# Performance work log

Measured on AMD Instinct MI355X. Metric: run time of the kernel, lower is better.

The kernel has to match this reference:

```python
import jax, jax.numpy as jnp
import numpy as np

N = 100000          # number of nodes (queries == sources here)
DEG = 32            # uniform neighbor count
E = N * DEG         # total edges
C_IN = 8
HID = 32
C_OUT = 32


def setup_inputs() -> dict:
    key = jax.random.key(0)
    k1, k2, k3, k4, k5 = jax.random.split(key, 5)
    in_features = jax.random.normal(k1, (N, C_IN), dtype=jnp.float32)
    in_weights = jax.random.uniform(k2, (N,), dtype=jnp.float32)
    # MLP: Linear(2*C_IN -> HID), GELU, Linear(HID -> C_OUT)
    W1 = jax.random.normal(k3, (2 * C_IN, HID), dtype=jnp.float32) / np.sqrt(2 * C_IN)
    b1 = jnp.zeros((HID,), dtype=jnp.float32)
    W2 = jax.random.normal(k4, (HID, C_OUT), dtype=jnp.float32) / np.sqrt(HID)
    b2 = jnp.zeros((C_OUT,), dtype=jnp.float32)
    neighbor_index = jax.random.randint(k5, (E,), 0, N, dtype=jnp.int64)
    row_splits = (jnp.arange(N + 1, dtype=jnp.int64) * DEG)  # uniform CSR splits
    return {"in_features": in_features, "in_weights": in_weights,
            "W1": W1, "b1": b1, "W2": W2, "b2": b2,
            "neighbor_index": neighbor_index, "row_splits": row_splits}


def reference(in_features, in_weights, W1, b1, W2, b2, neighbor_index, row_splits):
    num_edges = neighbor_index.shape[0]
    num_out = row_splits.shape[0] - 1  # M output nodes
    # segment id of each edge (== repeat_interleave of node ids by row counts)
    seg = jnp.searchsorted(row_splits, jnp.arange(num_edges), side="right") - 1
    gathered = in_features[neighbor_index]          # [E, C_in] neighbor gather
    self_feats = in_features[seg]                   # [E, C_in] repeated self features
    agg = jnp.concatenate([gathered, self_feats], axis=1)  # [E, 2*C_in]
    h = jax.nn.gelu(agg @ W1 + b1)                  # [E, HID]
    h = h @ W2 + b2                                 # [E, C_out]
    h = in_weights[neighbor_index][:, None] * h     # quadrature weighting
    sums = jax.ops.segment_sum(h, seg, num_segments=num_out)  # segment_csr sum
    counts = (row_splits[1:] - row_splits[:-1]).astype(h.dtype)
    out = sums / jnp.maximum(counts, 1)[:, None]    # reduce='mean'
    return out
```

## Files before the change

kernel.cpp:

```cpp
#include <hip/hip_runtime.h>

#define DEG 32
#define HID 32
#define CIN 8

typedef float v2f __attribute__((ext_vector_type(2)));

#define GELU_A ((float)(2.0 * 1.4426950408889634 * 0.7978845608028654))
#define GELU_B ((float)(2.0 * 1.4426950408889634 * 0.7978845608028654 * 0.044715))

__device__ __forceinline__ unsigned f2bf(float f) {
    unsigned b = __float_as_uint(f);
    return (b + 0x7fffu + ((b >> 16) & 1u)) >> 16;
}

__global__ __launch_bounds__(256) void precompute_u16(
    const float* __restrict__ x, const float* __restrict__ W1,
    unsigned* __restrict__ u16, int N) {
    int tid = blockIdx.x * 256 + threadIdx.x;
    if (tid >= N * 4) return;
    int n = tid >> 2;
    int q = tid & 3;
    const float4* xp = (const float4*)(x + (size_t)n * CIN);
    float4 a = xp[0], b = xp[1];
    float xv[8] = {a.x, a.y, a.z, a.w, b.x, b.y, b.z, b.w};
    float s[8];
#pragma unroll
    for (int c = 0; c < 8; ++c) s[c] = 0.f;
#pragma unroll
    for (int k = 0; k < 8; ++k) {
        float4 w0 = *(const float4*)(W1 + k * HID + q * 8);
        float4 w1 = *(const float4*)(W1 + k * HID + q * 8 + 4);
        s[0] = fmaf(xv[k], w0.x, s[0]); s[1] = fmaf(xv[k], w0.y, s[1]);
        s[2] = fmaf(xv[k], w0.z, s[2]); s[3] = fmaf(xv[k], w0.w, s[3]);
        s[4] = fmaf(xv[k], w1.x, s[4]); s[5] = fmaf(xv[k], w1.y, s[5]);
        s[6] = fmaf(xv[k], w1.z, s[6]); s[7] = fmaf(xv[k], w1.w, s[7]);
    }
    uint4 o;
    o.x = f2bf(s[0]) | (f2bf(s[1]) << 16);
    o.y = f2bf(s[2]) | (f2bf(s[3]) << 16);
    o.z = f2bf(s[4]) | (f2bf(s[5]) << 16);
    o.w = f2bf(s[6]) | (f2bf(s[7]) << 16);
    *(uint4*)(u16 + (size_t)n * 16 + q * 4) = o;
}

__global__ __launch_bounds__(256) void git_main3(
    const unsigned* __restrict__ u16, const float* __restrict__ x,
    const float* __restrict__ wgt, const float* __restrict__ W1,
    const float* __restrict__ b1, const float* __restrict__ W2,
    const float* __restrict__ b2, const int* __restrict__ nbr,
    float* __restrict__ out, int N) {
    __shared__ float sW2[HID * HID];
    __shared__ float sb2[HID];

    int t = threadIdx.x;
#pragma unroll
    for (int i = 0; i < 4; ++i) sW2[t + i * 256] = W2[t + i * 256];
    if (t < HID) sb2[t] = b2[t];

    int c2   = t & 15;
    int s    = (t >> 4) & 1;
    int slot = t >> 5;
    int node = blockIdx.x * 8 + slot;
    bool valid = node < N;
    int nc = valid ? node : (N - 1);

    int   j_own = nbr[nc * DEG + (t & 31)];
    int   off_l = j_own << 6;
    float w_own = wgt[j_own];

    float ws = w_own;
    ws += __shfl_xor(ws, 1);  ws += __shfl_xor(ws, 2);
    ws += __shfl_xor(ws, 4);  ws += __shfl_xor(ws, 8);
    ws += __shfl_xor(ws, 16);

    const float4* xip = (const float4*)(x + (size_t)nc * CIN);
    float4 xa = xip[0], xb = xip[1];
    float xs[8] = {xa.x, xa.y, xa.z, xa.w, xb.x, xb.y, xb.z, xb.w};
    v2f vb = *(const v2f*)(b1 + c2 * 2);
#pragma unroll
    for (int k = 0; k < 8; ++k) {
        v2f wcol = *(const v2f*)(W1 + (8 + k) * HID + c2 * 2);
        vb += xs[k] * wcol;
    }

    __syncthreads();

    const char* ub = (const char*)u16;
    int mybyte = c2 * 4;
    unsigned bits[16];
    float    wes[16];
#pragma unroll
    for (int e = 0; e < 16; ++e) {
        int src = 2 * e + s;
        int off = __shfl(off_l, src, 32);
        wes[e]  = __shfl(w_own, src, 32);
        bits[e] = *(const unsigned*)(ub + (unsigned)(off + mybyte));
    }

    v2f g = {0.f, 0.f};
#pragma unroll
    for (int e = 0; e < 16; ++e) {
        unsigned bb = bits[e];
        v2f uf;
        uf.x = __uint_as_float(bb << 16);
        uf.y = __uint_as_float(bb & 0xffff0000u);
        v2f tt = uf + vb;
        v2f x2 = tt * tt;
        v2f zz = tt * (x2 * GELU_B + GELU_A);
        v2f ee;
        ee.x = __builtin_amdgcn_exp2f(zz.x);
        ee.y = __builtin_amdgcn_exp2f(zz.y);
        v2f dd = ee + 1.0f;
        v2f rr;
        rr.x = __builtin_amdgcn_rcpf(dd.x);
        rr.y = __builtin_amdgcn_rcpf(dd.y);
        v2f gl = tt - tt * rr;
        g += wes[e] * gl;
    }

    g.x += __shfl_xor(g.x, 16);
    g.y += __shfl_xor(g.y, 16);

    v2f acc = {0.f, 0.f};
#pragma unroll
    for (int hh = 0; hh < 16; ++hh) {
        int h = s * 16 + hh;
        int srcl = s * 8 + (hh >> 1);
        float gh = (hh & 1) ? __shfl(g.y, srcl, 32) : __shfl(g.x, srcl, 32);
        v2f wrow = *(const v2f*)(sW2 + h * HID + c2 * 2);
        acc += gh * wrow;
    }
    acc.x += __shfl_xor(acc.x, 16);
    acc.y += __shfl_xor(acc.y, 16);

    if (valid && s == 0) {
        v2f bb2 = *(const v2f*)(sb2 + c2 * 2);
        v2f res = (acc + ws * bb2) * (1.0f / DEG);
        *(v2f*)(out + (size_t)node * HID + c2 * 2) = res;
    }
}

__global__ __launch_bounds__(256) void fused_fallback(
    const float* __restrict__ x, const float* __restrict__ wgt,
    const float* __restrict__ W1, const float* __restrict__ b1,
    const float* __restrict__ W2, const float* __restrict__ b2,
    const int* __restrict__ nbr, float* __restrict__ out, int N) {
    __shared__ float sW2[HID * HID];
    __shared__ float sb2[HID];
    __shared__ int2  sp[8 * DEG];
    int t = threadIdx.x;
#pragma unroll
    for (int i = 0; i < 4; ++i) sW2[t + i * 256] = W2[t + i * 256];
    if (t < HID) sb2[t] = b2[t];
    int slot = t >> 5, hid = t & 31;
    int node = blockIdx.x * 8 + slot;
    bool valid = node < N;
    int nc = valid ? node : (N - 1);
    int   j_own = nbr[nc * DEG + hid];
    float w_own = wgt[j_own];
    sp[slot * DEG + hid] = make_int2(j_own * (CIN * 4), __float_as_int(w_own));
    const float4* xip = (const float4*)(x + (size_t)nc * CIN);
    float4 xa = xip[0], xb = xip[1];
    float w1t[8];
#pragma unroll
    for (int k = 0; k < 8; ++k) w1t[k] = W1[k * HID + hid];
    float vb = b1[hid];
    vb = fmaf(xa.x, W1[ 8 * HID + hid], vb);
    vb = fmaf(xa.y, W1[ 9 * HID + hid], vb);
    vb = fmaf(xa.z, W1[10 * HID + hid], vb);
    vb = fmaf(xa.w, W1[11 * HID + hid], vb);
    vb = fmaf(xb.x, W1[12 * HID + hid], vb);
    vb = fmaf(xb.y, W1[13 * HID + hid], vb);
    vb = fmaf(xb.z, W1[14 * HID + hid], vb);
    vb = fmaf(xb.w, W1[15 * HID + hid], vb);
    float ws = w_own;
    ws += __shfl_xor(ws, 1);  ws += __shfl_xor(ws, 2);
    ws += __shfl_xor(ws, 4);  ws += __shfl_xor(ws, 8);
    ws += __shfl_xor(ws, 16);
    __syncthreads();
    const char* xbytes = (const char*)x;
    const int2* myp = &sp[slot * DEG];
    float g = 0.f;
#pragma unroll 8
    for (int e = 0; e < DEG; ++e) {
        int2  p  = myp[e];
        float wj = __int_as_float(p.y);
        const float4* xjp = (const float4*)(xbytes + (unsigned)p.x);
        float4 a = xjp[0], b = xjp[1];
        float tin = vb;
        tin = fmaf(a.x, w1t[0], tin); tin = fmaf(a.y, w1t[1], tin);
        tin = fmaf(a.z, w1t[2], tin); tin = fmaf(a.w, w1t[3], tin);
        tin = fmaf(b.x, w1t[4], tin); tin = fmaf(b.y, w1t[5], tin);
        tin = fmaf(b.z, w1t[6], tin); tin = fmaf(b.w, w1t[7], tin);
        float x2 = tin * tin;
        float z  = tin * fmaf(GELU_B, x2, GELU_A);
        float e2 = __builtin_amdgcn_exp2f(z);
        float r  = __builtin_amdgcn_rcpf(1.0f + e2);
        g = fmaf(wj, fmaf(-tin, r, tin), g);
    }
    float acc = 0.f;
#pragma unroll
    for (int h = 0; h < HID; ++h) {
        float gh = __shfl(g, h, 32);
        acc = fmaf(gh, sW2[h * HID + hid], acc);
    }
    if (valid) out[(size_t)node * HID + hid] = fmaf(ws, sb2[hid], acc) * (1.0f / DEG);
}

extern "C" void kernel_launch(void* const* d_in, const int* in_sizes, int n_in,
                              void* d_out, int out_size, void* d_ws, size_t ws_size,
                              hipStream_t stream) {
    const float* x   = (const float*)d_in[0];
    const float* wq  = (const float*)d_in[1];
    const float* W1  = (const float*)d_in[2];
    const float* b1  = (const float*)d_in[3];
    const float* W2  = (const float*)d_in[4];
    const float* b2  = (const float*)d_in[5];
    const int*   nbr = (const int*)d_in[6];
    float* out = (float*)d_out;

    int N = in_sizes[1];
    size_t need = (size_t)N * 64;

    if (ws_size >= need) {
        unsigned* u16 = (unsigned*)d_ws;
        int blocks_pre = (N * 4 + 255) / 256;
        precompute_u16<<<blocks_pre, 256, 0, stream>>>(x, W1, u16, N);
        int blocks_main = (N + 7) / 8;
        git_main3<<<blocks_main, 256, 0, stream>>>(u16, x, wq, W1, b1, W2, b2, nbr, out, N);
    } else {
        int blocks = (N + 7) / 8;
        fused_fallback<<<blocks, 256, 0, stream>>>(x, wq, W1, b1, W2, b2, nbr, out, N);
    }
}
```

Baseline: 132.3 us.

## Precompute self-projection per node and restructure gather to 8-byte loads via LDS

The prepass now also computes the self-feature half of the first layer plus bias (v = x·W1[8:16] + b1) per node in fp32 and stores it in the workspace, so the main kernel only loads it instead of recomputing it. The main kernel reworks the lane mapping: each lane handles 4 hidden channels for 8 edges and gathers 8-byte bf16 chunks, with neighbor offsets and weights passed through LDS instead of shuffles. The reduced g vector is staged in shared memory for the second-layer matmul, and launch bounds request 8 blocks per SM. In exchange the workspace needs an extra 128 bytes per node, which adds write and read traffic, and there are more cross-lane reductions.

Result: no change. 133.0 us (+0.6%).

```diff
diff --git a/kernel.cpp b/kernel.cpp
--- a/kernel.cpp
+++ b/kernel.cpp
@@ -14,9 +14,10 @@
     return (b + 0x7fffu + ((b >> 16) & 1u)) >> 16;
 }
 
-__global__ __launch_bounds__(256) void precompute_u16(
+__global__ __launch_bounds__(256) void precompute_uv16(
     const float* __restrict__ x, const float* __restrict__ W1,
-    unsigned* __restrict__ u16, int N) {
+    const float* __restrict__ b1, unsigned* __restrict__ u16,
+    float* __restrict__ v32, int N) {
     int tid = blockIdx.x * 256 + threadIdx.x;
     if (tid >= N * 4) return;
     int n = tid >> 2;
@@ -24,120 +25,140 @@
     const float4* xp = (const float4*)(x + (size_t)n * CIN);
     float4 a = xp[0], b = xp[1];
     float xv[8] = {a.x, a.y, a.z, a.w, b.x, b.y, b.z, b.w};
-    float s[8];
-#pragma unroll
-    for (int c = 0; c < 8; ++c) s[c] = 0.f;
+    float4 b1a = *(const float4*)(b1 + q * 8);
+    float4 b1b = *(const float4*)(b1 + q * 8 + 4);
+    float su[8] = {0.f, 0.f, 0.f, 0.f, 0.f, 0.f, 0.f, 0.f};
+    float sv[8] = {b1a.x, b1a.y, b1a.z, b1a.w, b1b.x, b1b.y, b1b.z, b1b.w};
 #pragma unroll
     for (int k = 0; k < 8; ++k) {
-        float4 w0 = *(const float4*)(W1 + k * HID + q * 8);
-        float4 w1 = *(const float4*)(W1 + k * HID + q * 8 + 4);
-        s[0] = fmaf(xv[k], w0.x, s[0]); s[1] = fmaf(xv[k], w0.y, s[1]);
-        s[2] = fmaf(xv[k], w0.z, s[2]); s[3] = fmaf(xv[k], w0.w, s[3]);
-        s[4] = fmaf(xv[k], w1.x, s[4]); s[5] = fmaf(xv[k], w1.y, s[5]);
-        s[6] = fmaf(xv[k], w1.z, s[6]); s[7] = fmaf(xv[k], w1.w, s[7]);
+        float4 u0 = *(const float4*)(W1 + k * HID + q * 8);
+        float4 u1 = *(const float4*)(W1 + k * HID + q * 8 + 4);
+        float4 v0 = *(const float4*)(W1 + (k + 8) * HID + q * 8);
+        float4 v1 = *(const float4*)(W1 + (k + 8) * HID + q * 8 + 4);
+        float xk = xv[k];
+        su[0] = fmaf(xk, u0.x, su[0]); su[1] = fmaf(xk, u0.y, su[1]);
+        su[2] = fmaf(xk, u0.z, su[2]); su[3] = fmaf(xk, u0.w, su[3]);
+        su[4] = fmaf(xk, u1.x, su[4]); su[5] = fmaf(xk, u1.y, su[5]);
+        su[6] = fmaf(xk, u1.z, su[6]); su[7] = fmaf(xk, u1.w, su[7]);
+        sv[0] = fmaf(xk, v0.x, sv[0]); sv[1] = fmaf(xk, v0.y, sv[1]);
+        sv[2] = fmaf(xk, v0.z, sv[2]); sv[3] = fmaf(xk, v0.w, sv[3]);
+        sv[4] = fmaf(xk, v1.x, sv[4]); sv[5] = fmaf(xk, v1.y, sv[5]);
+        sv[6] = fmaf(xk, v1.z, sv[6]); sv[7] = fmaf(xk, v1.w, sv[7]);
     }
     uint4 o;
-    o.x = f2bf(s[0]) | (f2bf(s[1]) << 16);
-    o.y = f2bf(s[2]) | (f2bf(s[3]) << 16);
-    o.z = f2bf(s[4]) | (f2bf(s[5]) << 16);
-    o.w = f2bf(s[6]) | (f2bf(s[7]) << 16);
+    o.x = f2bf(su[0]) | (f2bf(su[1]) << 16);
+    o.y = f2bf(su[2]) | (f2bf(su[3]) << 16);
+    o.z = f2bf(su[4]) | (f2bf(su[5]) << 16);
+    o.w = f2bf(su[6]) | (f2bf(su[7]) << 16);
     *(uint4*)(u16 + (size_t)n * 16 + q * 4) = o;
-}
-
-__global__ __launch_bounds__(256) void git_main3(
-    const unsigned* __restrict__ u16, const float* __restrict__ x,
-    const float* __restrict__ wgt, const float* __restrict__ W1,
-    const float* __restrict__ b1, const float* __restrict__ W2,
+    *(float4*)(v32 + (size_t)n * HID + q * 8)     = make_float4(sv[0], sv[1], sv[2], sv[3]);
+    *(float4*)(v32 + (size_t)n * HID + q * 8 + 4) = make_float4(sv[4], sv[5], sv[6], sv[7]);
+}
+
+__global__ __launch_bounds__(256, 8) void git_main4(
+    const unsigned* __restrict__ u16, const float* __restrict__ v32,
+    const float* __restrict__ wgt, const float* __restrict__ W2,
     const float* __restrict__ b2, const int* __restrict__ nbr,
     float* __restrict__ out, int N) {
     __shared__ float sW2[HID * HID];
     __shared__ float sb2[HID];
+    __shared__ int2  sp[8 * 33];
+    __shared__ float sg[8 * HID];
 
     int t = threadIdx.x;
 #pragma unroll
     for (int i = 0; i < 4; ++i) sW2[t + i * 256] = W2[t + i * 256];
     if (t < HID) sb2[t] = b2[t];
 
-    int c2   = t & 15;
-    int s    = (t >> 4) & 1;
     int slot = t >> 5;
+    int l5   = t & 31;
+    int ep   = l5 >> 3;
+    int c4   = l5 & 7;
     int node = blockIdx.x * 8 + slot;
     bool valid = node < N;
     int nc = valid ? node : (N - 1);
 
-    int   j_own = nbr[nc * DEG + (t & 31)];
-    int   off_l = j_own << 6;
+    int   j_own = nbr[nc * DEG + l5];
     float w_own = wgt[j_own];
+    sp[slot * 33 + l5] = make_int2(j_own << 6, __float_as_int(w_own));
 
     float ws = w_own;
     ws += __shfl_xor(ws, 1);  ws += __shfl_xor(ws, 2);
     ws += __shfl_xor(ws, 4);  ws += __shfl_xor(ws, 8);
     ws += __shfl_xor(ws, 16);
 
-    const float4* xip = (const float4*)(x + (size_t)nc * CIN);
-    float4 xa = xip[0], xb = xip[1];
-    float xs[8] = {xa.x, xa.y, xa.z, xa.w, xb.x, xb.y, xb.z, xb.w};
-    v2f vb = *(const v2f*)(b1 + c2 * 2);
-#pragma unroll
-    for (int k = 0; k < 8; ++k) {
-        v2f wcol = *(const v2f*)(W1 + (8 + k) * HID + c2 * 2);
-        vb += xs[k] * wcol;
-    }
+    float4 vv = *(const float4*)(v32 + (size_t)nc * HID + c4 * 4);
+    v2f vb0 = {vv.x, vv.y};
+    v2f vb1 = {vv.z, vv.w};
+
+    const int2* myp = &sp[slot * 33 + ep * 8];
+    const char* ub  = (const char*)u16;
+    int mybyte = c4 * 8;
+    uint2 bits[8];
+    float wj[8];
+#pragma unroll
+    for (int e = 0; e < 8; ++e) {
+        int2 p  = myp[e];
+        wj[e]   = __int_as_float(p.y);
+        bits[e] = *(const uint2*)(ub + (unsigned)(p.x + mybyte));
+    }
+
+    v2f g0 = {0.f, 0.f}, g1 = {0.f, 0.f};
+#pragma unroll
+    for (int e = 0; e < 8; ++e) {
+        unsigned ba = bits[e].x, bb = bits[e].y;
+        v2f uf0, uf1;
+        uf0.x = __uint_as_float(ba << 16);
+        uf0.y = __uint_as_float(ba & 0xffff0000u);
+        uf1.x = __uint_as_float(bb << 16);
+        uf1.y = __uint_as_float(bb & 0xffff0000u);
+        v2f t0 = uf0 + vb0, t1 = uf1 + vb1;
+        v2f x20 = t0 * t0,  x21 = t1 * t1;
+        v2f z0 = t0 * (x20 * GELU_B + GELU_A);
+        v2f z1 = t1 * (x21 * GELU_B + GELU_A);
+        v2f e0, e1;
+        e0.x = __builtin_amdgcn_exp2f(z0.x);  e0.y = __builtin_amdgcn_exp2f(z0.y);
+        e1.x = __builtin_amdgcn_exp2f(z1.x);  e1.y = __builtin_amdgcn_exp2f(z1.y);
+        v2f d0 = e0 + 1.0f, d1 = e1 + 1.0f;
+        v2f r0, r1;
+        r0.x = __builtin_amdgcn_rcpf(d0.x);  r0.y = __builtin_amdgcn_rcpf(d0.y);
+        r1.x = __builtin_amdgcn_rcpf(d1.x);  r1.y = __builtin_amdgcn_rcpf(d1.y);
+        v2f gl0 = t0 - t0 * r0;
+        v2f gl1 = t1 - t1 * r1;
+        g0 += wj[e] * gl0;
+        g1 += wj[e] * gl1;
+    }
+
+    g0.x += __shfl_xor(g0.x, 8);   g0.y += __shfl_xor(g0.y, 8);
+    g1.x += __shfl_xor(g1.x, 8);   g1.y += __shfl_xor(g1.y, 8);
+    g0.x += __shfl_xor(g0.x, 16);  g0.y += __shfl_xor(g0.y, 16);
+    g1.x += __shfl_xor(g1.x, 16);  g1.y += __shfl_xor(g1.y, 16);
+
+    if (l5 < 8)
+        *(float4*)(&sg[slot * HID + c4 * 4]) = make_float4(g0.x, g0.y, g1.x, g1.y);
 
     __syncthreads();
 
-    const char* ub = (const char*)u16;
-    int mybyte = c2 * 4;
-    unsigned bits[16];
-    float    wes[16];
-#pragma unroll
-    for (int e = 0; e < 16; ++e) {
-        int src = 2 * e + s;
-        int off = __shfl(off_l, src, 32);
-        wes[e]  = __shfl(w_own, src, 32);
-        bits[e] = *(const unsigned*)(ub + (unsigned)(off + mybyte));
-    }
-
-    v2f g = {0.f, 0.f};
-#pragma unroll
-    for (int e = 0; e < 16; ++e) {
-        unsigned bb = bits[e];
-        v2f uf;
-        uf.x = __uint_as_float(bb << 16);
-        uf.y = __uint_as_float(bb & 0xffff0000u);
-        v2f tt = uf + vb;
-        v2f x2 = tt * tt;
-        v2f zz = tt * (x2 * GELU_B + GELU_A);
-        v2f ee;
-        ee.x = __builtin_amdgcn_exp2f(zz.x);
-        ee.y = __builtin_amdgcn_exp2f(zz.y);
-        v2f dd = ee + 1.0f;
-        v2f rr;
-        rr.x = __builtin_amdgcn_rcpf(dd.x);
-        rr.y = __builtin_amdgcn_rcpf(dd.y);
-        v2f gl = tt - tt * rr;
-        g += wes[e] * gl;
-    }
-
-    g.x += __shfl_xor(g.x, 16);
-    g.y += __shfl_xor(g.y, 16);
-
+    int oc2 = l5 & 15;
+    int s   = l5 >> 4;
+    const float* sgrow  = &sg[slot * HID + s * 16];
+    const float* w2base = &sW2[(s * 16) * HID + oc2 * 2];
     v2f acc = {0.f, 0.f};
 #pragma unroll
-    for (int hh = 0; hh < 16; ++hh) {
-        int h = s * 16 + hh;
-        int srcl = s * 8 + (hh >> 1);
-        float gh = (hh & 1) ? __shfl(g.y, srcl, 32) : __shfl(g.x, srcl, 32);
-        v2f wrow = *(const v2f*)(sW2 + h * HID + c2 * 2);
-        acc += gh * wrow;
+    for (int hh = 0; hh < 8; ++hh) {
+        v2f gp = *(const v2f*)(sgrow + hh * 2);
+        v2f wa = *(const v2f*)(w2base + (hh * 2) * HID);
+        v2f wb = *(const v2f*)(w2base + (hh * 2 + 1) * HID);
+        acc += gp.x * wa;
+        acc += gp.y * wb;
     }
     acc.x += __shfl_xor(acc.x, 16);
     acc.y += __shfl_xor(acc.y, 16);
 
     if (valid && s == 0) {
-        v2f bb2 = *(const v2f*)(sb2 + c2 * 2);
+        v2f bb2 = *(const v2f*)(sb2 + oc2 * 2);
         v2f res = (acc + ws * bb2) * (1.0f / DEG);
-        *(v2f*)(out + (size_t)node * HID + c2 * 2) = res;
+        *(v2f*)(out + (size_t)node * HID + oc2 * 2) = res;
     }
 }
 
@@ -185,7 +206,7 @@
 #pragma unroll 8
     for (int e = 0; e < DEG; ++e) {
         int2  p  = myp[e];
-        float wj = __int_as_float(p.y);
+        float wjv = __int_as_float(p.y);
         const float4* xjp = (const float4*)(xbytes + (unsigned)p.x);
         float4 a = xjp[0], b = xjp[1];
         float tin = vb;
@@ -197,7 +218,7 @@
         float z  = tin * fmaf(GELU_B, x2, GELU_A);
         float e2 = __builtin_amdgcn_exp2f(z);
         float r  = __builtin_amdgcn_rcpf(1.0f + e2);
-        g = fmaf(wj, fmaf(-tin, r, tin), g);
+        g = fmaf(wjv, fmaf(-tin, r, tin), g);
     }
     float acc = 0.f;
 #pragma unroll
@@ -221,14 +242,15 @@
     float* out = (float*)d_out;
 
     int N = in_sizes[1];
-    size_t need = (size_t)N * 64;
+    size_t need = (size_t)N * (64 + 128);
 
     if (ws_size >= need) {
         unsigned* u16 = (unsigned*)d_ws;
+        float*    v32 = (float*)((char*)d_ws + (size_t)N * 64);
         int blocks_pre = (N * 4 + 255) / 256;
-        precompute_u16<<<blocks_pre, 256, 0, stream>>>(x, W1, u16, N);
+        precompute_uv16<<<blocks_pre, 256, 0, stream>>>(x, W1, b1, u16, v32, N);
         int blocks_main = (N + 7) / 8;
-        git_main3<<<blocks_main, 256, 0, stream>>>(u16, x, wq, W1, b1, W2, b2, nbr, out, N);
+        git_main4<<<blocks_main, 256, 0, stream>>>(u16, v32, wq, W2, b2, nbr, out, N);
     } else {
         int blocks = (N + 7) / 8;
         fused_fallback<<<blocks, 256, 0, stream>>>(x, wq, W1, b1, W2, b2, nbr, out, N);
```

## Compute first MLP layer per edge with bf16 MFMA on raw bf16 features

Applied to the files above, without the earlier changes.

Replaces the precomputed per-node x·W1 table (64 bytes per node) with a bf16 copy of the raw input features (16 bytes per node). The main kernel computes neighbor and self projections together with one 32x32x16 bf16 MFMA per wavefront. Each wavefront now handles one node instead of each 32-lane half handling one. This cuts gather traffic and moves the first layer onto matrix cores. The cost is fewer nodes per block and an extra LDS round trip for the second layer.

Measured after the change: 117.4 us. -11.2%, faster.

```diff
diff --git a/kernel.cpp b/kernel.cpp
--- a/kernel.cpp
+++ b/kernel.cpp
@@ -5,6 +5,8 @@
 #define CIN 8
 
 typedef float v2f __attribute__((ext_vector_type(2)));
+typedef short bf16x8 __attribute__((ext_vector_type(8)));
+typedef float f32x16 __attribute__((ext_vector_type(16)));
 
 #define GELU_A ((float)(2.0 * 1.4426950408889634 * 0.7978845608028654))
 #define GELU_B ((float)(2.0 * 1.4426950408889634 * 0.7978845608028654 * 0.044715))
@@ -13,132 +15,117 @@
     unsigned b = __float_as_uint(f);
     return (b + 0x7fffu + ((b >> 16) & 1u)) >> 16;
 }
-
-__global__ __launch_bounds__(256) void precompute_u16(
+__device__ __forceinline__ unsigned pack2(float lo, float hi) {
+    return f2bf(lo) | (f2bf(hi) << 16);
+}
+
+__global__ __launch_bounds__(256) void precompute_xw(
     const float* __restrict__ x, const float* __restrict__ W1,
-    unsigned* __restrict__ u16, int N) {
+    unsigned* __restrict__ x16, unsigned* __restrict__ w1f, int N) {
     int tid = blockIdx.x * 256 + threadIdx.x;
-    if (tid >= N * 4) return;
-    int n = tid >> 2;
-    int q = tid & 3;
-    const float4* xp = (const float4*)(x + (size_t)n * CIN);
-    float4 a = xp[0], b = xp[1];
-    float xv[8] = {a.x, a.y, a.z, a.w, b.x, b.y, b.z, b.w};
-    float s[8];
-#pragma unroll
-    for (int c = 0; c < 8; ++c) s[c] = 0.f;
-#pragma unroll
-    for (int k = 0; k < 8; ++k) {
-        float4 w0 = *(const float4*)(W1 + k * HID + q * 8);
-        float4 w1 = *(const float4*)(W1 + k * HID + q * 8 + 4);
-        s[0] = fmaf(xv[k], w0.x, s[0]); s[1] = fmaf(xv[k], w0.y, s[1]);
-        s[2] = fmaf(xv[k], w0.z, s[2]); s[3] = fmaf(xv[k], w0.w, s[3]);
-        s[4] = fmaf(xv[k], w1.x, s[4]); s[5] = fmaf(xv[k], w1.y, s[5]);
-        s[6] = fmaf(xv[k], w1.z, s[6]); s[7] = fmaf(xv[k], w1.w, s[7]);
-    }
-    uint4 o;
-    o.x = f2bf(s[0]) | (f2bf(s[1]) << 16);
-    o.y = f2bf(s[2]) | (f2bf(s[3]) << 16);
-    o.z = f2bf(s[4]) | (f2bf(s[5]) << 16);
-    o.w = f2bf(s[6]) | (f2bf(s[7]) << 16);
-    *(uint4*)(u16 + (size_t)n * 16 + q * 4) = o;
-}
-
-__global__ __launch_bounds__(256) void git_main3(
-    const unsigned* __restrict__ u16, const float* __restrict__ x,
-    const float* __restrict__ wgt, const float* __restrict__ W1,
-    const float* __restrict__ b1, const float* __restrict__ W2,
-    const float* __restrict__ b2, const int* __restrict__ nbr,
-    float* __restrict__ out, int N) {
+    if (blockIdx.x == 0 && threadIdx.x < 64) {
+        int l  = threadIdx.x;
+        int kb = (l >> 5) * 8;
+        int col = l & 31;
+        uint4 o;
+        o.x = pack2(W1[(kb + 0) * HID + col], W1[(kb + 1) * HID + col]);
+        o.y = pack2(W1[(kb + 2) * HID + col], W1[(kb + 3) * HID + col]);
+        o.z = pack2(W1[(kb + 4) * HID + col], W1[(kb + 5) * HID + col]);
+        o.w = pack2(W1[(kb + 6) * HID + col], W1[(kb + 7) * HID + col]);
+        *(uint4*)(w1f + l * 4) = o;
+    }
+    if (tid < N) {
+        const float4* xp = (const float4*)(x + (size_t)tid * CIN);
+        float4 a = xp[0], b = xp[1];
+        uint4 o;
+        o.x = pack2(a.x, a.y);  o.y = pack2(a.z, a.w);
+        o.z = pack2(b.x, b.y);  o.w = pack2(b.z, b.w);
+        *(uint4*)(x16 + (size_t)tid * 4) = o;
+    }
+}
+
+__global__ __launch_bounds__(256) void git_mfma(
+    const unsigned* __restrict__ x16, const unsigned* __restrict__ w1f,
+    const float* __restrict__ wgt, const float* __restrict__ b1,
+    const float* __restrict__ W2, const float* __restrict__ b2,
+    const int* __restrict__ nbr, float* __restrict__ out, int N) {
     __shared__ float sW2[HID * HID];
-    __shared__ float sb2[HID];
+    __shared__ float sw[4 * DEG];
+    __shared__ float sg[4 * HID];
 
     int t = threadIdx.x;
 #pragma unroll
     for (int i = 0; i < 4; ++i) sW2[t + i * 256] = W2[t + i * 256];
-    if (t < HID) sb2[t] = b2[t];
-
-    int c2   = t & 15;
-    int s    = (t >> 4) & 1;
-    int slot = t >> 5;
-    int node = blockIdx.x * 8 + slot;
-    bool valid = node < N;
-    int nc = valid ? node : (N - 1);
-
-    int   j_own = nbr[nc * DEG + (t & 31)];
-    int   off_l = j_own << 6;
-    float w_own = wgt[j_own];
-
-    float ws = w_own;
+
+    int wv = t >> 6;
+    int l  = t & 63;
+    int l5 = l & 31;
+    int hi = l >> 5;
+    int node = blockIdx.x * 4 + wv;
+    int nc = node < N ? node : (N - 1);
+
+    int   jn = nbr[nc * DEG + l5];
+    float w  = wgt[jn];
+    if (hi == 0) sw[wv * DEG + l5] = w;
+
+    float ws = w;
     ws += __shfl_xor(ws, 1);  ws += __shfl_xor(ws, 2);
     ws += __shfl_xor(ws, 4);  ws += __shfl_xor(ws, 8);
     ws += __shfl_xor(ws, 16);
 
-    const float4* xip = (const float4*)(x + (size_t)nc * CIN);
-    float4 xa = xip[0], xb = xip[1];
-    float xs[8] = {xa.x, xa.y, xa.z, xa.w, xb.x, xb.y, xb.z, xb.w};
-    v2f vb = *(const v2f*)(b1 + c2 * 2);
-#pragma unroll
-    for (int k = 0; k < 8; ++k) {
-        v2f wcol = *(const v2f*)(W1 + (8 + k) * HID + c2 * 2);
-        vb += xs[k] * wcol;
-    }
-
-    __syncthreads();
-
-    const char* ub = (const char*)u16;
-    int mybyte = c2 * 4;
-    unsigned bits[16];
-    float    wes[16];
-#pragma unroll
-    for (int e = 0; e < 16; ++e) {
-        int src = 2 * e + s;
-        int off = __shfl(off_l, src, 32);
-        wes[e]  = __shfl(w_own, src, 32);
-        bits[e] = *(const unsigned*)(ub + (unsigned)(off + mybyte));
-    }
-
-    v2f g = {0.f, 0.f};
-#pragma unroll
-    for (int e = 0; e < 16; ++e) {
-        unsigned bb = bits[e];
-        v2f uf;
-        uf.x = __uint_as_float(bb << 16);
-        uf.y = __uint_as_float(bb & 0xffff0000u);
-        v2f tt = uf + vb;
+    int arow = hi ? nc : jn;
+    bf16x8 af = *((const bf16x8*)x16 + arow);
+    bf16x8 bf = *((const bf16x8*)w1f + l);
+    float myb1 = b1[l5];
+
+    f32x16 acc = {};
+    acc = __builtin_amdgcn_mfma_f32_32x32x16_bf16(af, bf, acc, 0, 0, 0);
+
+    int base = hi * 4;
+    const float* swp = &sw[wv * DEG + base];
+    float4 wq0 = *(const float4*)(swp);
+    float4 wq1 = *(const float4*)(swp + 8);
+    float4 wq2 = *(const float4*)(swp + 16);
+    float4 wq3 = *(const float4*)(swp + 24);
+    float wqa[16] = {wq0.x, wq0.y, wq0.z, wq0.w,  wq1.x, wq1.y, wq1.z, wq1.w,
+                     wq2.x, wq2.y, wq2.z, wq2.w,  wq3.x, wq3.y, wq3.z, wq3.w};
+
+    float g = 0.f;
+#pragma unroll
+    for (int i = 0; i < 16; i += 2) {
+        v2f tt = {acc[i] + myb1, acc[i + 1] + myb1};
         v2f x2 = tt * tt;
         v2f zz = tt * (x2 * GELU_B + GELU_A);
         v2f ee;
-        ee.x = __builtin_amdgcn_exp2f(zz.x);
-        ee.y = __builtin_amdgcn_exp2f(zz.y);
+        ee.x = __builtin_amdgcn_exp2f(zz.x);  ee.y = __builtin_amdgcn_exp2f(zz.y);
         v2f dd = ee + 1.0f;
         v2f rr;
-        rr.x = __builtin_amdgcn_rcpf(dd.x);
-        rr.y = __builtin_amdgcn_rcpf(dd.y);
+        rr.x = __builtin_amdgcn_rcpf(dd.x);   rr.y = __builtin_amdgcn_rcpf(dd.y);
         v2f gl = tt - tt * rr;
-        g += wes[e] * gl;
-    }
-
-    g.x += __shfl_xor(g.x, 16);
-    g.y += __shfl_xor(g.y, 16);
-
-    v2f acc = {0.f, 0.f};
-#pragma unroll
-    for (int hh = 0; hh < 16; ++hh) {
-        int h = s * 16 + hh;
-        int srcl = s * 8 + (hh >> 1);
-        float gh = (hh & 1) ? __shfl(g.y, srcl, 32) : __shfl(g.x, srcl, 32);
-        v2f wrow = *(const v2f*)(sW2 + h * HID + c2 * 2);
-        acc += gh * wrow;
-    }
-    acc.x += __shfl_xor(acc.x, 16);
-    acc.y += __shfl_xor(acc.y, 16);
-
-    if (valid && s == 0) {
-        v2f bb2 = *(const v2f*)(sb2 + c2 * 2);
-        v2f res = (acc + ws * bb2) * (1.0f / DEG);
-        *(v2f*)(out + (size_t)node * HID + c2 * 2) = res;
-    }
+        g = fmaf(wqa[i],     gl.x, g);
+        g = fmaf(wqa[i + 1], gl.y, g);
+    }
+    g += __shfl_xor(g, 32);
+    if (hi == 0) sg[wv * HID + l5] = g;
+
+    __syncthreads();
+
+    const float* gp  = &sg[wv * HID + hi * 16];
+    const float* w2p = &sW2[(hi * 16) * HID + l5];
+    float4 g0 = *(const float4*)(gp);
+    float4 g1 = *(const float4*)(gp + 4);
+    float4 g2 = *(const float4*)(gp + 8);
+    float4 g3 = *(const float4*)(gp + 12);
+    float ga[16] = {g0.x, g0.y, g0.z, g0.w,  g1.x, g1.y, g1.z, g1.w,
+                    g2.x, g2.y, g2.z, g2.w,  g3.x, g3.y, g3.z, g3.w};
+    float acc2 = 0.f;
+#pragma unroll
+    for (int h = 0; h < 16; ++h)
+        acc2 = fmaf(ga[h], w2p[h * HID], acc2);
+    acc2 += __shfl_xor(acc2, 32);
+
+    if (node < N && hi == 0)
+        out[(size_t)node * HID + l5] = fmaf(ws, b2[l5], acc2) * (1.0f / DEG);
 }
 
 __global__ __launch_bounds__(256) void fused_fallback(
@@ -185,7 +172,7 @@
 #pragma unroll 8
     for (int e = 0; e < DEG; ++e) {
         int2  p  = myp[e];
-        float wj = __int_as_float(p.y);
+        float wjv = __int_as_float(p.y);
         const float4* xjp = (const float4*)(xbytes + (unsigned)p.x);
         float4 a = xjp[0], b = xjp[1];
         float tin = vb;
@@ -197,7 +184,7 @@
         float z  = tin * fmaf(GELU_B, x2, GELU_A);
         float e2 = __builtin_amdgcn_exp2f(z);
         float r  = __builtin_amdgcn_rcpf(1.0f + e2);
-        g = fmaf(wj, fmaf(-tin, r, tin), g);
+        g = fmaf(wjv, fmaf(-tin, r, tin), g);
     }
     float acc = 0.f;
 #pragma unroll
@@ -221,14 +208,15 @@
     float* out = (float*)d_out;
 
     int N = in_sizes[1];
-    size_t need = (size_t)N * 64;
+    size_t need = (size_t)N * 16 + 1024;
 
     if (ws_size >= need) {
-        unsigned* u16 = (unsigned*)d_ws;
-        int blocks_pre = (N * 4 + 255) / 256;
-        precompute_u16<<<blocks_pre, 256, 0, stream>>>(x, W1, u16, N);
-        int blocks_main = (N + 7) / 8;
-        git_main3<<<blocks_main, 256, 0, stream>>>(u16, x, wq, W1, b1, W2, b2, nbr, out, N);
+        unsigned* x16 = (unsigned*)d_ws;
+        unsigned* w1f = (unsigned*)((char*)d_ws + (size_t)N * 16);
+        int blocks_pre = (N + 255) / 256;
+        precompute_xw<<<blocks_pre, 256, 0, stream>>>(x, W1, x16, w1f, N);
+        int blocks_main = (N + 3) / 4;
+        git_mfma<<<blocks_main, 256, 0, stream>>>(x16, w1f, wq, b1, W2, b2, nbr, out, N);
     } else {
         int blocks = (N + 7) / 8;
         fused_fallback<<<blocks, 256, 0, stream>>>(x, wq, W1, b1, W2, b2, nbr, out, N);
```
